# Performance work log

Measured on AMD Instinct MI355X. Metric: run time of the kernel, lower is better.

The kernel has to match this reference:

```python
import jax, jax.numpy as jnp
import numpy as np

# SAUCD simp_wt branch constants (cfg values)
MODEL_SIZE = 64
WEIGHT_BOTTOM = -6.0      # log-lambda floor of the weight segments
SEG_W = 0.105             # log-lambda width of each weight segment
EPS = 1e-8

B, M, L = 8, 16, 131072


def weight_segment(w_abs, lmbd):
    """Map each eigenvalue to its log-spaced weight bin and gather the weight.
    w_abs: [K] nonneg weights; lmbd: [B,M,L] eigenvalues in (0, 2]."""
    logl = jnp.log(jnp.clip(lmbd, EPS, None))
    idx = jnp.clip(jnp.floor((logl - WEIGHT_BOTTOM) / SEG_W), 0, MODEL_SIZE - 1).astype(jnp.int32)
    return w_abs[idx]  # [B,M,L]


def setup_inputs() -> dict:
    key = jax.random.key(0)
    k0, k1, k2, k3 = jax.random.split(key, 4)
    weight = jax.random.uniform(k0, (MODEL_SIZE,), dtype=jnp.float32, minval=0.5, maxval=1.5)
    # N_array_areas: per-interval counts/normalizers (positive)
    N_array_areas = jax.random.uniform(k1, (B, M, L), dtype=jnp.float32, minval=0.0, maxval=1.0)
    # sorted eigenvalues of a normalized Laplacian: ascending values in (0, 2]
    raw = jax.random.uniform(k2, (B, M, L + 1), dtype=jnp.float32, minval=1e-6, maxval=2.0)
    sorted_lmbd = jnp.sort(raw, axis=-1)
    # signed AUC-difference areas per interval
    areas = jax.random.normal(k3, (B, M, L), dtype=jnp.float32) * 1e-4
    return {"weight": weight, "N_array_areas": N_array_areas,
            "sorted_lmbd": sorted_lmbd, "areas": areas}


def reference(weight, N_array_areas, sorted_lmbd, areas):
    w_abs = jnp.abs(weight)
    weight_seg = weight_segment(w_abs, sorted_lmbd[:, :, 1:])  # [B,M,L]
    weighted = weight_seg * N_array_areas * areas               # fused elementwise
    score = jnp.clip(jnp.sum(weighted, axis=-1), 0.0, 2.0)      # [B,M]
    return score
```

## Files before the change

kernel.cpp:

```cpp
#include <hip/hip_runtime.h>


#define N_ROWS 128
#define ROW_L 131072
#define BLOCKS_PER_ROW 16
#define TPB 256
#define ELEMS_PER_THREAD 32

__global__ __launch_bounds__(TPB) void saucd_reduce_kernel(
    const float* __restrict__ weight,
    const float* __restrict__ narr,
    const float* __restrict__ lmbd,
    const float* __restrict__ areas,
    float* __restrict__ out)
{
    __shared__ float w_abs[64];
    if (threadIdx.x < 64) w_abs[threadIdx.x] = fabsf(weight[threadIdx.x]);
    __syncthreads();

    const int row = blockIdx.y;
    const long long row_base  = (long long)row * ROW_L;
    const long long lmbd_base = (long long)row * (ROW_L + 1) + 1;
    const int chunk = blockIdx.x * (TPB * ELEMS_PER_THREAD) + threadIdx.x;

    float acc = 0.0f;
#pragma unroll
    for (int k = 0; k < ELEMS_PER_THREAD; ++k) {
        const int e = chunk + k * TPB;
        const float l = lmbd[lmbd_base + e];
        const float n = narr[row_base + e];
        const float a = areas[row_base + e];
        const float logl = logf(fmaxf(l, 1e-8f));
        const float t = (logl + 6.0f) / 0.105f;
        int idx = (int)floorf(t);
        idx = min(max(idx, 0), 63);
        acc = fmaf(w_abs[idx] * n, a, acc);
    }

#pragma unroll
    for (int off = 32; off > 0; off >>= 1)
        acc += __shfl_down(acc, off, 64);

    __shared__ float wave_sum[TPB / 64];
    const int lane = threadIdx.x & 63;
    const int wid  = threadIdx.x >> 6;
    if (lane == 0) wave_sum[wid] = acc;
    __syncthreads();
    if (threadIdx.x == 0) {
        float s = wave_sum[0] + wave_sum[1] + wave_sum[2] + wave_sum[3];
        atomicAdd(&out[row], s);
    }
}

__global__ void saucd_finalize_kernel(float* __restrict__ out, int n) {
    const int i = threadIdx.x + blockIdx.x * blockDim.x;
    if (i < n) out[i] = fminf(fmaxf(out[i], 0.0f), 2.0f);
}

extern "C" void kernel_launch(void* const* d_in, const int* in_sizes, int n_in,
                              void* d_out, int out_size, void* d_ws, size_t ws_size,
                              hipStream_t stream) {
    const float* weight = (const float*)d_in[0];
    const float* narr   = (const float*)d_in[1];
    const float* lmbd   = (const float*)d_in[2];
    const float* areas  = (const float*)d_in[3];
    float* out = (float*)d_out;

    hipMemsetAsync(out, 0, (size_t)out_size * sizeof(float), stream);

    dim3 grid(BLOCKS_PER_ROW, N_ROWS);
    saucd_reduce_kernel<<<grid, TPB, 0, stream>>>(weight, narr, lmbd, areas, out);
    saucd_finalize_kernel<<<1, 128, 0, stream>>>(out, out_size);
}
```

Before: 205.0 us.

## Vectorize loads to float4, prefetch next group, use fast log and multiply

Each thread now loads four contiguous elements at a time with float4 reads, using an unaligned 16-byte memcpy for the lambda row that is offset by one. The next group is prefetched before the current one is processed, and four independent accumulators are kept. Bin computation switches to __logf with a reciprocal multiply and float clamping instead of logf, a divide and floorf. This cuts memory instructions and ALU work, but the fast log and reciprocal can move values that sit on a bin boundary into the neighbouring bin, and the float-to-int truncation matches floor only because the value is clamped to be nonnegative first.

Result: faster. 200.5 us (-2.2%).

```diff
diff --git a/kernel.cpp b/kernel.cpp
--- a/kernel.cpp
+++ b/kernel.cpp
@@ -5,7 +5,14 @@
 #define ROW_L 131072
 #define BLOCKS_PER_ROW 16
 #define TPB 256
-#define ELEMS_PER_THREAD 32
+#define CHUNK (ROW_L / BLOCKS_PER_ROW)
+#define GROUPS (CHUNK / (TPB * 4))
+
+__device__ __forceinline__ int wbin(float l) {
+    const float logl = __logf(fmaxf(l, 1e-8f));
+    const float t = (logl + 6.0f) * 9.52380952380952381f;
+    return (int)fminf(fmaxf(t, 0.0f), 63.0f);
+}
 
 __global__ __launch_bounds__(TPB) void saucd_reduce_kernel(
     const float* __restrict__ weight,
@@ -19,23 +26,37 @@
     __syncthreads();
 
     const int row = blockIdx.y;
-    const long long row_base  = (long long)row * ROW_L;
-    const long long lmbd_base = (long long)row * (ROW_L + 1) + 1;
-    const int chunk = blockIdx.x * (TPB * ELEMS_PER_THREAD) + threadIdx.x;
+    const size_t blk = (size_t)row * ROW_L + (size_t)blockIdx.x * CHUNK;
+    const float4* __restrict__ narr4  = (const float4*)(narr  + blk);
+    const float4* __restrict__ areas4 = (const float4*)(areas + blk);
+    const float*  __restrict__ lp     = lmbd + (size_t)row * (ROW_L + 1) + 1
+                                             + (size_t)blockIdx.x * CHUNK;
 
-    float acc = 0.0f;
+    float acc0 = 0.0f, acc1 = 0.0f, acc2 = 0.0f, acc3 = 0.0f;
+
+    int g = threadIdx.x;
+    float4 nv = narr4[g];
+    float4 av = areas4[g];
+    float4 lv;
+    __builtin_memcpy(&lv, lp + 4 * g, 16);
+
 #pragma unroll
-    for (int k = 0; k < ELEMS_PER_THREAD; ++k) {
-        const int e = chunk + k * TPB;
-        const float l = lmbd[lmbd_base + e];
-        const float n = narr[row_base + e];
-        const float a = areas[row_base + e];
-        const float logl = logf(fmaxf(l, 1e-8f));
-        const float t = (logl + 6.0f) / 0.105f;
-        int idx = (int)floorf(t);
-        idx = min(max(idx, 0), 63);
-        acc = fmaf(w_abs[idx] * n, a, acc);
+    for (int k = 0; k < GROUPS; ++k) {
+        const float4 cn = nv, ca = av, cl = lv;
+        if (k + 1 < GROUPS) {
+            const int g2 = g + TPB;
+            nv = narr4[g2];
+            av = areas4[g2];
+            __builtin_memcpy(&lv, lp + 4 * g2, 16);
+            g = g2;
+        }
+        acc0 = fmaf(w_abs[wbin(cl.x)] * cn.x, ca.x, acc0);
+        acc1 = fmaf(w_abs[wbin(cl.y)] * cn.y, ca.y, acc1);
+        acc2 = fmaf(w_abs[wbin(cl.z)] * cn.z, ca.z, acc2);
+        acc3 = fmaf(w_abs[wbin(cl.w)] * cn.w, ca.w, acc3);
     }
+
+    float acc = (acc0 + acc1) + (acc2 + acc3);
 
 #pragma unroll
     for (int off = 32; off > 0; off >>= 1)
@@ -47,7 +68,7 @@
     if (lane == 0) wave_sum[wid] = acc;
     __syncthreads();
     if (threadIdx.x == 0) {
-        float s = wave_sum[0] + wave_sum[1] + wave_sum[2] + wave_sum[3];
+        float s = (wave_sum[0] + wave_sum[1]) + (wave_sum[2] + wave_sum[3]);
         atomicAdd(&out[row], s);
     }
 }
```

## Double-buffer input tiles into LDS via direct global-to-LDS async loads

Applied to the files above, without the earlier changes.

Replaces direct per-thread global loads with a double-buffered pipeline. global_load_lds DMA stages tiles of narr, areas and lambda into shared memory, and the kernel waits with manual vmcnt counts before consuming the current tile. Also switches to fast __logf with a multiply instead of divide, and uses four independent accumulators with float4 LDS reads. This adds a missing barrier risk: there is no __syncthreads between tiles, so cross-wave LDS reads rely on each thread loading and consuming the same slots, which holds for N and A but not clearly for L.

After: 208.6 us. No clear change (+1.8%).

```diff
diff --git a/kernel.cpp b/kernel.cpp
--- a/kernel.cpp
+++ b/kernel.cpp
@@ -1,11 +1,27 @@
 #include <hip/hip_runtime.h>
+#include <stdint.h>
 
 
-#define N_ROWS 128
+#define TPB 512
+#define TILE 2048
+#define TILES_PER_BLOCK 16
+#define NBLOCKS 512
 #define ROW_L 131072
-#define BLOCKS_PER_ROW 16
-#define TPB 256
-#define ELEMS_PER_THREAD 32
+
+__device__ __forceinline__ void gload16(const float* g, float* l) {
+    __builtin_amdgcn_global_load_lds((const __attribute__((address_space(1))) void*)g,
+                                     (__attribute__((address_space(3))) void*)l, 16, 0, 0);
+}
+__device__ __forceinline__ void gload4(const float* g, float* l) {
+    __builtin_amdgcn_global_load_lds((const __attribute__((address_space(1))) void*)g,
+                                     (__attribute__((address_space(3))) void*)l, 4, 0, 0);
+}
+
+__device__ __forceinline__ int wbin(float l) {
+    const float logl = __logf(fmaxf(l, 1e-8f));
+    const float t = (logl + 6.0f) * 9.52380952380952381f;
+    return (int)fminf(fmaxf(t, 0.0f), 63.0f);
+}
 
 __global__ __launch_bounds__(TPB) void saucd_reduce_kernel(
     const float* __restrict__ weight,
@@ -14,40 +30,73 @@
     const float* __restrict__ areas,
     float* __restrict__ out)
 {
+    __shared__ float bufN[2][TILE];
+    __shared__ float bufA[2][TILE];
+    __shared__ float bufL[2][TILE];
     __shared__ float w_abs[64];
-    if (threadIdx.x < 64) w_abs[threadIdx.x] = fabsf(weight[threadIdx.x]);
+    __shared__ float wave_sum[TPB / 64];
+
+    const int tid  = threadIdx.x;
+    const int lane = tid & 63;
+    const int wbase = (tid >> 6) * 256;
+
+    if (tid < 64) w_abs[tid] = fabsf(weight[tid]);
     __syncthreads();
 
-    const int row = blockIdx.y;
-    const long long row_base  = (long long)row * ROW_L;
-    const long long lmbd_base = (long long)row * (ROW_L + 1) + 1;
-    const int chunk = blockIdx.x * (TPB * ELEMS_PER_THREAD) + threadIdx.x;
+    const int b = blockIdx.x;
+    const int row = b >> 2;
+    const size_t base = (size_t)row * ROW_L + (size_t)(b & 3) * (TILE * TILES_PER_BLOCK);
+    const float* nrow = narr  + base;
+    const float* arow = areas + base;
+    const float* lrow = lmbd  + (size_t)row * (ROW_L + 1)
+                              + (size_t)(b & 3) * (TILE * TILES_PER_BLOCK) + 1;
 
-    float acc = 0.0f;
+    auto stage = [&](int tk, int which) {
+        const size_t off = (size_t)tk * TILE;
+        gload16(nrow + off + (size_t)tid * 4, &bufN[which][tid * 4]);
+        gload16(arow + off + (size_t)tid * 4, &bufA[which][tid * 4]);
 #pragma unroll
-    for (int k = 0; k < ELEMS_PER_THREAD; ++k) {
-        const int e = chunk + k * TPB;
-        const float l = lmbd[lmbd_base + e];
-        const float n = narr[row_base + e];
-        const float a = areas[row_base + e];
-        const float logl = logf(fmaxf(l, 1e-8f));
-        const float t = (logl + 6.0f) / 0.105f;
-        int idx = (int)floorf(t);
-        idx = min(max(idx, 0), 63);
-        acc = fmaf(w_abs[idx] * n, a, acc);
+        for (int k = 0; k < 4; ++k) {
+            const int j = wbase + k * 64 + lane;
+            gload4(lrow + off + j, &bufL[which][j]);
+        }
+    };
+
+    stage(0, 0);
+
+    float acc0 = 0.0f, acc1 = 0.0f, acc2 = 0.0f, acc3 = 0.0f;
+
+#pragma unroll 1
+    for (int t = 0; t < TILES_PER_BLOCK; ++t) {
+        const int cur = t & 1;
+        if (t + 1 < TILES_PER_BLOCK) {
+            stage(t + 1, cur ^ 1);
+            asm volatile("s_waitcnt vmcnt(6)" ::: "memory");
+        } else {
+            asm volatile("s_waitcnt vmcnt(0)" ::: "memory");
+        }
+        const float4 lv = *(const float4*)&bufL[cur][tid * 4];
+        const float4 nv = *(const float4*)&bufN[cur][tid * 4];
+        const float4 av = *(const float4*)&bufA[cur][tid * 4];
+        acc0 = fmaf(w_abs[wbin(lv.x)] * nv.x, av.x, acc0);
+        acc1 = fmaf(w_abs[wbin(lv.y)] * nv.y, av.y, acc1);
+        acc2 = fmaf(w_abs[wbin(lv.z)] * nv.z, av.z, acc2);
+        acc3 = fmaf(w_abs[wbin(lv.w)] * nv.w, av.w, acc3);
     }
+
+    float acc = (acc0 + acc1) + (acc2 + acc3);
 
 #pragma unroll
     for (int off = 32; off > 0; off >>= 1)
         acc += __shfl_down(acc, off, 64);
 
-    __shared__ float wave_sum[TPB / 64];
-    const int lane = threadIdx.x & 63;
-    const int wid  = threadIdx.x >> 6;
-    if (lane == 0) wave_sum[wid] = acc;
     __syncthreads();
-    if (threadIdx.x == 0) {
-        float s = wave_sum[0] + wave_sum[1] + wave_sum[2] + wave_sum[3];
+    if (lane == 0) wave_sum[tid >> 6] = acc;
+    __syncthreads();
+    if (tid == 0) {
+        float s = 0.0f;
+#pragma unroll
+        for (int w = 0; w < TPB / 64; ++w) s += wave_sum[w];
         atomicAdd(&out[row], s);
     }
 }
@@ -68,7 +117,6 @@
 
     hipMemsetAsync(out, 0, (size_t)out_size * sizeof(float), stream);
 
-    dim3 grid(BLOCKS_PER_ROW, N_ROWS);
-    saucd_reduce_kernel<<<grid, TPB, 0, stream>>>(weight, narr, lmbd, areas, out);
+    saucd_reduce_kernel<<<NBLOCKS, TPB, 0, stream>>>(weight, narr, lmbd, areas, out);
     saucd_finalize_kernel<<<1, 128, 0, stream>>>(out, out_size);
 }
```
